# Kernel optimization log

Hardware: AMD Instinct MI355X
Metric: run time of the kernel (lower is better)

The kernel has to match this reference:

```python
import math
import jax, jax.numpy as jnp
import numpy as np

# ---- Clifford algebra Cl(1,3) tables (static, built in numpy) ----
DIM = 4
METRIC = np.array([1.0, -1.0, -1.0, -1.0], dtype=np.float64)
N_COMP = 1 << DIM  # 16 multivector components
SUBSPACES = np.array([math.comb(DIM, g) for g in range(DIM + 1)])  # [1,4,6,4,1]

def _popcount(x):
    return bin(x).count("1")

# blades ordered by (grade, bitmask) as in CGENN-style algebras
_BLADES = sorted(range(N_COMP), key=lambda b: (_popcount(b), b))
_IDX = {b: i for i, b in enumerate(_BLADES)}

def _blade_prod(a, b):
    # canonical reordering sign
    s, t = 0, a >> 1
    while t:
        s += _popcount(t & b)
        t >>= 1
    sign = -1.0 if (s % 2) else 1.0
    for i in range(DIM):
        if (a >> i) & 1 and (b >> i) & 1:
            sign *= METRIC[i]
    return a ^ b, sign

# cayley[i, j, k]: coefficient of e_j in e_i * e_k  (matches einsum '...i,ijk,...k->...j')
CAYLEY = np.zeros((N_COMP, N_COMP, N_COMP), dtype=np.float32)
for a in range(N_COMP):
    for b in range(N_COMP):
        c, s = _blade_prod(a, b)
        CAYLEY[_IDX[a], _IDX[c], _IDX[b]] = s

GRADES = np.array([_popcount(b) for b in _BLADES])
BETA = np.array([float(np.prod([METRIC[i] for i in range(DIM) if (b >> i) & 1])) for b in _BLADES], dtype=np.float32)  # blade quadratic-form signs
GRADE_ONEHOT = (GRADES[:, None] == np.arange(DIM + 1)[None, :]).astype(np.float32)  # [16,5]

_sl = np.concatenate([[0], np.cumsum(SUBSPACES)])
PATHS = np.zeros((DIM + 1,) * 3, dtype=bool)
for i in range(DIM + 1):
    for j in range(DIM + 1):
        for k in range(DIM + 1):
            PATHS[i, j, k] = np.any(CAYLEY[_sl[i]:_sl[i+1], _sl[j]:_sl[j+1], _sl[k]:_sl[k+1]] != 0)
PI, PJ, PK = np.nonzero(PATHS)
N_PATHS = int(PATHS.sum())  # 35 for Cl(1,3)
EPS = 1e-6


def mvlinear(x, w):
    # x: [b, m, 16], w: [n, m, 5] (one scalar weight per grade) -> [b, n, 16]
    w16 = jnp.repeat(w, SUBSPACES, axis=-1)  # [n, m, 16]
    return jnp.einsum('bmi,nmi->bni', x, w16)


def normalize(x, a):
    # per-grade norm: |b(x_g, x_g)|^0.5, gated by sigmoid(a)
    q = ((x * x) * BETA) @ GRADE_ONEHOT            # [b, n, 5]
    norms = jnp.sqrt(jnp.abs(q))
    norms = jax.nn.sigmoid(a) * (norms - 1.0) + 1.0
    norms16 = jnp.repeat(norms, SUBSPACES, axis=-1)  # [b, n, 16]
    return x / (norms16 + EPS)


def get_weight(gp_weight):
    # scatter [F, 35] params into [F,5,5,5], expand to [F,16,16,16], mask by Cayley
    F = gp_weight.shape[0]
    w = jnp.zeros((F, DIM + 1, DIM + 1, DIM + 1), gp_weight.dtype).at[:, PI, PJ, PK].set(gp_weight)
    w = jnp.repeat(w, SUBSPACES, axis=1)
    w = jnp.repeat(w, SUBSPACES, axis=2)
    w = jnp.repeat(w, SUBSPACES, axis=3)
    return jnp.asarray(CAYLEY) * w  # [F,16,16,16]


def setup_inputs() -> dict:
    key = jax.random.key(0)
    k0, k1, k2, k3, k4 = jax.random.split(key, 5)
    B, F = 4096, 512
    x = jax.random.normal(k0, (B, F, N_COMP), jnp.float32)
    s = 1.0 / math.sqrt(F)
    w_left = jax.random.normal(k1, (F, F, DIM + 1), jnp.float32) * s
    b_left = jax.random.normal(k2, (F,), jnp.float32) * 0.01
    w_right = jax.random.normal(k3, (F, F, DIM + 1), jnp.float32) * s
    a_norm = jnp.zeros((F, DIM + 1), jnp.float32)  # normalization_init = 0
    gp_weight = jax.random.normal(k4, (F, N_PATHS), jnp.float32) * (1.0 / math.sqrt(DIM + 1))
    return {"x": x, "w_left": w_left, "b_left": b_left, "w_right": w_right,
            "a_norm": a_norm, "gp_weight": gp_weight}


def reference(x, w_left, b_left, w_right, a_norm, gp_weight):
    input_right = normalize(mvlinear(x, w_right), a_norm)
    W = get_weight(gp_weight)                       # [F,16,16,16]
    gp = jnp.einsum('bni,nijk,bnk->bnj', x, W, input_right)
    left = mvlinear(x, w_left).at[..., 0].add(b_left)  # bias embedded at grade-0 component
    return (left + gp) / math.sqrt(2.0)
```

## Files before the change

kernel.cpp:

```cpp
#include <hip/hip_runtime.h>

typedef unsigned int uint;
typedef unsigned short ushort;
typedef __attribute__((ext_vector_type(8))) short bf16x8;
typedef __attribute__((ext_vector_type(4))) float f32x4;

struct GPTables {
    signed char jid[16][16];
    float       sgn[16][16];
    signed char pid[16][16];
    float       beta[16];
    signed char grade[16];
};

constexpr int popc4(int x) { return ((x >> 0) & 1) + ((x >> 1) & 1) + ((x >> 2) & 1) + ((x >> 3) & 1); }

constexpr GPTables make_tables() {
    GPTables T{};
    int blades[16] = {0, 1, 2, 4, 8, 3, 5, 6, 9, 10, 12, 7, 11, 13, 14, 15};
    int idxof[16] = {};
    for (int i = 0; i < 16; ++i) idxof[blades[i]] = i;
    float metric[4] = {1.f, -1.f, -1.f, -1.f};
    for (int i = 0; i < 16; ++i) {
        T.grade[i] = (signed char)popc4(blades[i]);
        float b = 1.f;
        for (int bit = 0; bit < 4; ++bit)
            if ((blades[i] >> bit) & 1) b *= metric[bit];
        T.beta[i] = b;
    }
    bool paths[5][5][5] = {};
    for (int a = 0; a < 16; ++a)
        for (int b = 0; b < 16; ++b)
            paths[popc4(a)][popc4(a ^ b)][popc4(b)] = true;
    int pid3[5][5][5] = {};
    int cnt = 0;
    for (int gi = 0; gi < 5; ++gi)
        for (int gj = 0; gj < 5; ++gj)
            for (int gk = 0; gk < 5; ++gk)
                if (paths[gi][gj][gk]) pid3[gi][gj][gk] = cnt++;
    for (int ii = 0; ii < 16; ++ii) {
        for (int kk = 0; kk < 16; ++kk) {
            int a = blades[ii], b = blades[kk];
            int c = a ^ b;
            int s = 0, t = a >> 1;
            while (t) { s += popc4(t & b); t >>= 1; }
            float sign = (s & 1) ? -1.f : 1.f;
            for (int bit = 0; bit < 4; ++bit)
                if (((a >> bit) & 1) && ((b >> bit) & 1)) sign *= metric[bit];
            T.jid[ii][kk] = (signed char)idxof[c];
            T.sgn[ii][kk] = sign;
            T.pid[ii][kk] = (signed char)pid3[popc4(a)][popc4(c)][popc4(b)];
        }
    }
    return T;
}

constexpr GPTables TBL = make_tables();

#define BF (4096)
#define FF (512)
#define BM_ (2097152)
#define FFFF (262144)

__device__ inline ushort f2bf(float f) {
    uint u = __float_as_uint(f);
    uint r = (u + 0x7fffu + ((u >> 16) & 1u)) >> 16;
    return (ushort)r;
}
__device__ inline float bf2f(ushort h) { return __uint_as_float(((uint)h) << 16); }

typedef __attribute__((address_space(3))) uint lds_u32;
typedef const __attribute__((address_space(1))) uint g_u32;
__device__ __forceinline__ void gload16(const void* gsrc, void* ldst) {
    __builtin_amdgcn_global_load_lds((g_u32*)gsrc, (lds_u32*)ldst, 16, 0, 0);
}

__global__ __launch_bounds__(256) void k_transpose_x(const float* __restrict__ x,
                                                     ushort* __restrict__ Xh,
                                                     ushort* __restrict__ Xl) {
    const int p0 = (blockIdx.x * 256 + threadIdx.x) * 2;
    float v[32];
    const float4* x4 = (const float4*)(x + (size_t)p0 * 16);
#pragma unroll
    for (int j = 0; j < 8; ++j) {
        float4 t = x4[j];
        v[j * 4 + 0] = t.x; v[j * 4 + 1] = t.y; v[j * 4 + 2] = t.z; v[j * 4 + 3] = t.w;
    }
#pragma unroll
    for (int i = 0; i < 16; ++i) {
        ushort h0 = f2bf(v[i]),      h1 = f2bf(v[16 + i]);
        ushort l0 = f2bf(v[i] - bf2f(h0));
        ushort l1 = f2bf(v[16 + i] - bf2f(h1));
        *(uint*)&Xh[(size_t)i * BM_ + p0] = (uint)h0 | ((uint)h1 << 16);
        *(uint*)&Xl[(size_t)i * BM_ + p0] = (uint)l0 | ((uint)l1 << 16);
    }
}

__global__ __launch_bounds__(256) void k_prep_w(const float* __restrict__ w_right,
                                                const float* __restrict__ w_left,
                                                ushort* __restrict__ Wb) {
    const int n = blockIdx.x;
    const int m = threadIdx.x * 2;
#pragma unroll
    for (int g = 0; g < 5; ++g) {
        float a = w_right[(size_t)n * (FF * 5) + (size_t)m * 5 + g];
        float b = w_right[(size_t)n * (FF * 5) + (size_t)(m + 1) * 5 + g];
        ushort ah = f2bf(a), bh = f2bf(b);
        ushort al = f2bf(a - bf2f(ah)), bl = f2bf(b - bf2f(bh));
        *(uint*)&Wb[(size_t)g * FFFF + (size_t)n * FF + m] = (uint)ah | ((uint)bh << 16);
        *(uint*)&Wb[(size_t)(5 + g) * FFFF + (size_t)n * FF + m] = (uint)al | ((uint)bl << 16);
        float c = w_left[(size_t)n * (FF * 5) + (size_t)m * 5 + g];
        float d = w_left[(size_t)n * (FF * 5) + (size_t)(m + 1) * 5 + g];
        *(uint*)&Wb[(size_t)(10 + g) * FFFF + (size_t)n * FF + m] =
            (uint)f2bf(c) | ((uint)f2bf(d) << 16);
    }
}

__device__ __forceinline__ bf16x8 ldfrag(const ushort* tile, int row, int colb) {
    return *(const bf16x8*)((const char*)tile + row * 64 + (colb ^ ((row & 3) << 4)));
}

__global__ __launch_bounds__(256, 2) void k_gemm(const ushort* __restrict__ Xh,
                                                 const ushort* __restrict__ Xl,
                                                 const ushort* __restrict__ Wb,
                                                 float* __restrict__ OutR,
                                                 ushort* __restrict__ OutL) {
    const int comp = blockIdx.z;
    const int g = TBL.grade[comp];
    const ushort* Ah = Xh + (size_t)comp * BM_;
    const ushort* Al = Xl + (size_t)comp * BM_;
    const ushort* Bh = Wb + (size_t)g * FFFF;
    const ushort* Bl = Wb + (size_t)(5 + g) * FFFF;
    const ushort* BL = Wb + (size_t)(10 + g) * FFFF;
    const int m0 = blockIdx.x * 128;
    const int n0 = blockIdx.y * 128;

    __shared__ ushort sh[5 * 128 * 32];
    ushort* tA  = sh;
    ushort* tAl = sh + 1 * 4096;
    ushort* tBh = sh + 2 * 4096;
    ushort* tBl = sh + 3 * 4096;
    ushort* tBL = sh + 4 * 4096;

    const int tid = threadIdx.x;
    const int lane = tid & 63, wid = tid >> 6;
    const int wm = wid >> 1, wn = wid & 1;
    const int lr = lane & 15;
    const int kb = (lane >> 4) * 16;

    f32x4 accR[4][4] = {};
    f32x4 accL[4][4] = {};

    for (int k0 = 0; k0 < FF; k0 += 32) {
#pragma unroll
        for (int pass = 0; pass < 2; ++pass) {
            const int c = tid + pass * 256;
            const int row = c >> 2;
            const int scb = ((c & 3) * 16) ^ ((row & 3) << 4);
            const size_t gb = (size_t)row * (FF * 2) + (size_t)k0 * 2 + scb;
            const size_t mb_ = (size_t)m0 * (FF * 2), nb_ = (size_t)n0 * (FF * 2);
            char* dst = (char*)sh + c * 16;
            gload16((const char*)Ah + mb_ + gb, dst);
            gload16((const char*)Al + mb_ + gb, dst + 8192);
            gload16((const char*)Bh + nb_ + gb, dst + 16384);
            gload16((const char*)Bl + nb_ + gb, dst + 24576);
            gload16((const char*)BL + nb_ + gb, dst + 32768);
        }
        __syncthreads();
        bf16x8 ah[4], al[4], bh[4], bl[4], bLf[4];
#pragma unroll
        for (int mb = 0; mb < 4; ++mb) {
            ah[mb] = ldfrag(tA,  wm * 64 + mb * 16 + lr, kb);
            al[mb] = ldfrag(tAl, wm * 64 + mb * 16 + lr, kb);
        }
#pragma unroll
        for (int nb = 0; nb < 4; ++nb) {
            bh[nb]  = ldfrag(tBh, wn * 64 + nb * 16 + lr, kb);
            bl[nb]  = ldfrag(tBl, wn * 64 + nb * 16 + lr, kb);
            bLf[nb] = ldfrag(tBL, wn * 64 + nb * 16 + lr, kb);
        }
#pragma unroll
        for (int mb = 0; mb < 4; ++mb)
#pragma unroll
            for (int nb = 0; nb < 4; ++nb) {
                accR[mb][nb] = __builtin_amdgcn_mfma_f32_16x16x32_bf16(ah[mb], bh[nb],  accR[mb][nb], 0, 0, 0);
                accR[mb][nb] = __builtin_amdgcn_mfma_f32_16x16x32_bf16(ah[mb], bl[nb],  accR[mb][nb], 0, 0, 0);
                accR[mb][nb] = __builtin_amdgcn_mfma_f32_16x16x32_bf16(al[mb], bh[nb],  accR[mb][nb], 0, 0, 0);
                accL[mb][nb] = __builtin_amdgcn_mfma_f32_16x16x32_bf16(ah[mb], bLf[nb], accL[mb][nb], 0, 0, 0);
            }
        __syncthreads();
    }

    float* CR = OutR + (size_t)comp * BM_;
    ushort* CL = OutL + (size_t)comp * BM_;
#pragma unroll
    for (int mb = 0; mb < 4; ++mb)
#pragma unroll
        for (int nb = 0; nb < 4; ++nb) {
            int row = m0 + wm * 64 + mb * 16 + (lane >> 4) * 4;
            int col = n0 + wn * 64 + nb * 16 + (lane & 15);
#pragma unroll
            for (int r = 0; r < 4; ++r) {
                CR[(size_t)(row + r) * FF + col] = accR[mb][nb][r];
                CL[(size_t)(row + r) * FF + col] = f2bf(accL[mb][nb][r]);
            }
        }
}

__global__ __launch_bounds__(256) void k_gp(const float* __restrict__ x,
                                            const float* __restrict__ OutR,
                                            const ushort* __restrict__ OutL,
                                            const float* __restrict__ gpw,
                                            const float* __restrict__ a_norm,
                                            const float* __restrict__ b_left,
                                            float* __restrict__ out) {
    __shared__ float s_pw[256 * 35];
    __shared__ float s_an[256 * 5];
    __shared__ float s_bl[256];

    const int tid = threadIdx.x;
    const int bn = blockIdx.x * 256 + tid;
    const int n0 = (blockIdx.x & 1) * 256;

    for (int i = tid; i < 256 * 35; i += 256) s_pw[i] = gpw[(size_t)n0 * 35 + i];
#pragma unroll
    for (int i = 0; i < 5; ++i) s_an[tid + i * 256] = a_norm[(size_t)n0 * 5 + tid + i * 256];
    s_bl[tid] = b_left[n0 + tid];
    __syncthreads();

    float xi[16];
    {
        const float4* xp = (const float4*)(x + (size_t)bn * 16);
#pragma unroll
        for (int j = 0; j < 4; ++j) {
            float4 t = xp[j];
            xi[j * 4 + 0] = t.x; xi[j * 4 + 1] = t.y; xi[j * 4 + 2] = t.z; xi[j * 4 + 3] = t.w;
        }
    }

    float R[16];
#pragma unroll
    for (int i = 0; i < 16; ++i) R[i] = OutR[(size_t)i * BM_ + bn];

    float q[5] = {0.f, 0.f, 0.f, 0.f, 0.f};
#pragma unroll
    for (int i = 0; i < 16; ++i) q[TBL.grade[i]] += TBL.beta[i] * R[i] * R[i];
    float inv[5];
#pragma unroll
    for (int g = 0; g < 5; ++g) {
        float nr = sqrtf(fabsf(q[g]));
        float a = s_an[tid * 5 + g];
        float sig = 1.f / (1.f + __expf(-a));
        float nf = sig * (nr - 1.f) + 1.f + 1e-6f;
        inv[g] = 1.f / nf;
    }
#pragma unroll
    for (int i = 0; i < 16; ++i) R[i] *= inv[TBL.grade[i]];

    float pw[35];
#pragma unroll
    for (int p = 0; p < 35; ++p) pw[p] = s_pw[tid * 35 + p];

    float acc[16] = {};
#pragma unroll
    for (int ii = 0; ii < 16; ++ii) {
#pragma unroll
        for (int kk = 0; kk < 16; ++kk) {
            const int j = TBL.jid[ii][kk];
            const int p = TBL.pid[ii][kk];
            const float s = TBL.sgn[ii][kk];
            acc[j] += (s * pw[p]) * (xi[ii] * R[kk]);
        }
    }

    const float bl = s_bl[tid];
    float o[16];
#pragma unroll
    for (int j = 0; j < 16; ++j) {
        float l = bf2f(OutL[(size_t)j * BM_ + bn]);
        if (j == 0) l += bl;
        o[j] = (l + acc[j]) * 0.70710678118654752440f;
    }
    float4* op = (float4*)(out + (size_t)bn * 16);
#pragma unroll
    for (int j = 0; j < 4; ++j) {
        float4 t;
        t.x = o[j * 4 + 0]; t.y = o[j * 4 + 1]; t.z = o[j * 4 + 2]; t.w = o[j * 4 + 3];
        op[j] = t;
    }
}

extern "C" void kernel_launch(void* const* d_in, const int* in_sizes, int n_in,
                              void* d_out, int out_size, void* d_ws, size_t ws_size,
                              hipStream_t stream) {
    (void)in_sizes; (void)n_in; (void)out_size; (void)ws_size;
    const float* x       = (const float*)d_in[0];
    const float* w_left  = (const float*)d_in[1];
    const float* b_left  = (const float*)d_in[2];
    const float* w_right = (const float*)d_in[3];
    const float* a_norm  = (const float*)d_in[4];
    const float* gpw     = (const float*)d_in[5];
    float* out = (float*)d_out;

    char* ws = (char*)d_ws;
    ushort* Xh   = (ushort*)ws;
    ushort* Xl   = (ushort*)(ws + 67108864);
    ushort* Wb   = (ushort*)(ws + 134217728);
    float*  OutR = (float*)(ws + 142082048);
    ushort* OutL = (ushort*)(ws + 276299776);

    k_transpose_x<<<4096, 256, 0, stream>>>(x, Xh, Xl);
    k_prep_w<<<512, 256, 0, stream>>>(w_right, w_left, Wb);
    dim3 g(32, 4, 16);
    k_gemm<<<g, 256, 0, stream>>>(Xh, Xl, Wb, OutR, OutL);
    k_gp<<<8192, 256, 0, stream>>>(x, OutR, OutL, gpw, a_norm, b_left, out);
}
```

Baseline: 367.4 us.

## Double-buffer GEMM LDS tiles, adjust swizzle, and read x from bf16 planes in k_gp

The GEMM main loop now uses two LDS buffers, loading the next 32-wide K slice while MFMAs run on the current one. The goal is to hide global-load latency behind compute. The LDS swizzle XOR changes from row&3 to (row>>2)&3 to cut bank conflicts on fragment reads. k_gp now rebuilds x from the component-major bf16 hi/lo planes with coalesced loads instead of strided fp32 float4 reads. The costs are doubled LDS use per block (80KB, which limits occupancy to two blocks per CU) and a slight precision loss from the bf16 hi+lo reconstruction of x.

```diff
diff --git a/kernel.cpp b/kernel.cpp
--- a/kernel.cpp
+++ b/kernel.cpp
@@ -117,7 +117,7 @@
 }
 
 __device__ __forceinline__ bf16x8 ldfrag(const ushort* tile, int row, int colb) {
-    return *(const bf16x8*)((const char*)tile + row * 64 + (colb ^ ((row & 3) << 4)));
+    return *(const bf16x8*)((const char*)tile + row * 64 + (colb ^ (((row >> 2) & 3) << 4)));
 }
 
 __global__ __launch_bounds__(256, 2) void k_gemm(const ushort* __restrict__ Xh,
@@ -135,12 +135,7 @@
     const int m0 = blockIdx.x * 128;
     const int n0 = blockIdx.y * 128;
 
-    __shared__ ushort sh[5 * 128 * 32];
-    ushort* tA  = sh;
-    ushort* tAl = sh + 1 * 4096;
-    ushort* tBh = sh + 2 * 4096;
-    ushort* tBl = sh + 3 * 4096;
-    ushort* tBL = sh + 4 * 4096;
+    __shared__ ushort sh[2 * 5 * 4096];
 
     const int tid = threadIdx.x;
     const int lane = tid & 63, wid = tid >> 6;
@@ -148,25 +143,40 @@
     const int lr = lane & 15;
     const int kb = (lane >> 4) * 16;
 
-    f32x4 accR[4][4] = {};
-    f32x4 accL[4][4] = {};
-
-    for (int k0 = 0; k0 < FF; k0 += 32) {
+    const size_t mb_ = (size_t)m0 * (FF * 2), nb_ = (size_t)n0 * (FF * 2);
+
+    auto stage = [&](int buf, int k0) {
 #pragma unroll
         for (int pass = 0; pass < 2; ++pass) {
             const int c = tid + pass * 256;
             const int row = c >> 2;
-            const int scb = ((c & 3) * 16) ^ ((row & 3) << 4);
+            const int scb = ((c & 3) * 16) ^ (((c >> 4) & 3) << 4);
             const size_t gb = (size_t)row * (FF * 2) + (size_t)k0 * 2 + scb;
-            const size_t mb_ = (size_t)m0 * (FF * 2), nb_ = (size_t)n0 * (FF * 2);
-            char* dst = (char*)sh + c * 16;
+            char* dst = (char*)sh + buf * 40960 + c * 16;
             gload16((const char*)Ah + mb_ + gb, dst);
             gload16((const char*)Al + mb_ + gb, dst + 8192);
             gload16((const char*)Bh + nb_ + gb, dst + 16384);
             gload16((const char*)Bl + nb_ + gb, dst + 24576);
             gload16((const char*)BL + nb_ + gb, dst + 32768);
         }
-        __syncthreads();
+    };
+
+    f32x4 accR[4][4] = {};
+    f32x4 accL[4][4] = {};
+
+    stage(0, 0);
+    __syncthreads();
+
+    for (int t = 0; t < 16; ++t) {
+        const ushort* sb = sh + (t & 1) * 20480;
+        if (t < 15) stage((t + 1) & 1, (t + 1) * 32);
+
+        const ushort* tA  = sb;
+        const ushort* tAl = sb + 1 * 4096;
+        const ushort* tBh = sb + 2 * 4096;
+        const ushort* tBl = sb + 3 * 4096;
+        const ushort* tBL = sb + 4 * 4096;
+
         bf16x8 ah[4], al[4], bh[4], bl[4], bLf[4];
 #pragma unroll
         for (int mb = 0; mb < 4; ++mb) {
@@ -207,7 +217,8 @@
         }
 }
 
-__global__ __launch_bounds__(256) void k_gp(const float* __restrict__ x,
+__global__ __launch_bounds__(256) void k_gp(const ushort* __restrict__ Xh,
+                                            const ushort* __restrict__ Xl,
                                             const float* __restrict__ OutR,
                                             const ushort* __restrict__ OutL,
                                             const float* __restrict__ gpw,
@@ -229,14 +240,9 @@
     __syncthreads();
 
     float xi[16];
-    {
-        const float4* xp = (const float4*)(x + (size_t)bn * 16);
-#pragma unroll
-        for (int j = 0; j < 4; ++j) {
-            float4 t = xp[j];
-            xi[j * 4 + 0] = t.x; xi[j * 4 + 1] = t.y; xi[j * 4 + 2] = t.z; xi[j * 4 + 3] = t.w;
-        }
-    }
+#pragma unroll
+    for (int i = 0; i < 16; ++i)
+        xi[i] = bf2f(Xh[(size_t)i * BM_ + bn]) + bf2f(Xl[(size_t)i * BM_ + bn]);
 
     float R[16];
 #pragma unroll
@@ -313,5 +319,5 @@
     k_prep_w<<<512, 256, 0, stream>>>(w_right, w_left, Wb);
     dim3 g(32, 4, 16);
     k_gemm<<<g, 256, 0, stream>>>(Xh, Xl, Wb, OutR, OutL);
-    k_gp<<<8192, 256, 0, stream>>>(x, OutR, OutL, gpw, a_norm, b_left, out);
-}
+    k_gp<<<8192, 256, 0, stream>>>(Xh, Xl, OutR, OutL, gpw, a_norm, b_left, out);
+}
```

New measurement: 407.4 us. +10.9%, slower.
